# Optimization experiments

Hardware: AMD Instinct MI355X
Metric: run time of the kernel (lower is better)

## Reference

```python
import jax, jax.numpy as jnp
import numpy as np

B, T, H, W = 4, 8, 256, 256


def _shift(u, axis, d):
    """Value at index i comes from i+d along `axis`; zero (Dirichlet) boundary."""
    if d == 0:
        return u
    pad = [(0, 0)] * u.ndim
    sl = [slice(None)] * u.ndim
    if d > 0:
        sl[axis] = slice(d, None)
        pad[axis] = (0, d)
    else:
        sl[axis] = slice(None, d)
        pad[axis] = (-d, 0)
    return jnp.pad(u[tuple(sl)], pad)


def custom_sigmoid(x, mn, mx):
    # matches NLL.custom_sigmoid: (sigmoid(x) + min/(max-min)) * (max-min)
    return (jax.nn.sigmoid(x) + mn / (mx - mn)) * (mx - mn)


def setup_inputs() -> dict:
    key = jax.random.key(0)
    k1, k2 = jax.random.split(key)
    x = jax.random.normal(k1, (B, T, H, W), dtype=jnp.float32)
    conv_w = jax.random.normal(k2, (8 * T, T, 3, 3), dtype=jnp.float32) * 0.05
    return {"x": x, "conv_w": conv_w}


def reference(x, conv_w):
    Bn, Tn, Hn, Wn = x.shape
    dt = dx = dy = 1.0  # st_lag = [1,1,1]

    # Encoder: Conv2d(n_t -> 8*n_t, 3x3, padding=1, bias=False)
    theta = jax.lax.conv_general_dilated(
        x, conv_w, window_strides=(1, 1), padding="SAME",
        dimension_numbers=("NCHW", "OIHW", "NCHW"))

    # reshape_params: split 8*n_t channels into SPDE fields, bounded to valid ranges
    kappa = custom_sigmoid(theta[:, :Tn], 0.01, 1.0)          # damping
    m1 = theta[:, Tn:2 * Tn]                                   # advection x
    m2 = theta[:, 2 * Tn:3 * Tn]                               # advection y
    Hxx = custom_sigmoid(theta[:, 3 * Tn:4 * Tn], 0.01, 1.0)  # diffusion tensor
    Hxy = 0.1 * jnp.tanh(theta[:, 4 * Tn:5 * Tn])
    Hyx = 0.1 * jnp.tanh(theta[:, 5 * Tn:6 * Tn])
    Hyy = custom_sigmoid(theta[:, 6 * Tn:7 * Tn], 0.01, 1.0)
    tau = custom_sigmoid(theta[:, 7 * Tn:8 * Tn], 0.1, 10.0)   # noise scale

    # finite-difference stencils (zero Dirichlet boundary), vectorized over (B,T)
    def Dx(u):
        return (_shift(u, -1, 1) - _shift(u, -1, -1)) / (2 * dx)

    def Dy(u):
        return (_shift(u, -2, 1) - _shift(u, -2, -1)) / (2 * dy)

    def Dxx(u):
        return (_shift(u, -1, 1) + _shift(u, -1, -1) - 2 * u) / (dx * dx)

    def Dyy(u):
        return (_shift(u, -2, 1) + _shift(u, -2, -1) - 2 * u) / (dy * dy)

    def A(u):
        # advection-diffusion operator: kappa^2 u + m.grad u - div(H grad u)
        return ((kappa * kappa) * u + m1 * Dx(u) + m2 * Dy(u)
                - (Hxx * Dxx(u) + Hyy * Dyy(u) + (Hxy + Hyx) * Dx(Dy(u))))

    # pow=1 -> alpha=2 -> B = A^2 ; M_k = I + dt * B_k
    Mx = x + dt * A(A(x))                      # [B,T,H,W], M_k x_k for all k

    # Q = L^T D L with L block-bidiagonal (L[k,k]=M_k, L[k,k-1]=-I),
    # D_k = diag(dt / tau_k^2)  (inv_tau = sqrt(dt)/tau in create_Q)
    x_prev = jnp.concatenate([jnp.zeros_like(x[:, :1]), x[:, :-1]], axis=1)
    r = Mx - x_prev                            # r_k = M_k x_k - x_{k-1}
    D = dt / (tau * tau)

    xQx = jnp.sum(D * r * r)                   # quadratic form x^T Q x
    logdetD = jnp.sum(jnp.log(D))              # diagonal log-det contribution
    return 0.5 * (xQx - logdetD)
```

## Files before the change

kernel.cpp:

```cpp
#include <hip/hip_runtime.h>

#define F_ELEMS 2097152
#define IMG 65536

typedef _Float16 half8  __attribute__((ext_vector_type(8)));
typedef _Float16 half2v __attribute__((ext_vector_type(2)));
typedef _Float16 half4v __attribute__((ext_vector_type(4)));
typedef float    floatx4 __attribute__((ext_vector_type(4)));

__device__ __forceinline__ float sigm(float x){ return 1.0f/(1.0f + __expf(-x)); }
__device__ __forceinline__ float tanh_fast(float x){
    float t = __expf(2.0f*x);
    return 1.0f - 2.0f/(t + 1.0f);
}

__global__ void zero_out(float* out){ out[0] = 0.0f; }

__global__ __launch_bounds__(256) void conv_mfma(
    const float* __restrict__ x, const float* __restrict__ w,
    _Float16* __restrict__ fld, float* __restrict__ out)
{
    __shared__ _Float16 xt[4*258*8];
    __shared__ _Float16 Wl[12*64*8];
    __shared__ float red[256];

    const int tid = threadIdx.x;
    const int i0  = blockIdx.x << 1;
    const int b   = blockIdx.y;

    for (int e = tid; e < 258*4*4; e += 256){
        int cc = e % 258;
        int rr = (e/258) & 3;
        int cp = e / (258*4);
        int gi = i0 - 1 + rr, gj = cc - 1;
        float v0 = 0.0f, v1 = 0.0f;
        if (gi >= 0 && gi < 256 && gj >= 0 && gj < 256){
            int base = ((b*8 + 2*cp) << 16) + (gi << 8) + gj;
            v0 = x[base];
            v1 = x[base + IMG];
        }
        half2v h; h[0] = (_Float16)v0; h[1] = (_Float16)v1;
        *(half2v*)&xt[(rr*258 + cc)*8 + 2*cp] = h;
    }
    for (int e = tid; e < 12*64*8; e += 256){
        int c  = e & 7;
        int oc = (e >> 3) & 63;
        int t  = e >> 9;
        float v = (t < 9) ? w[(oc*8 + c)*9 + t] : 0.0f;
        Wl[e] = (_Float16)v;
    }
    __syncthreads();

    const int lane = tid & 63;
    const int quad = lane >> 4;
    const int l16  = lane & 15;
    const int wv   = tid >> 6;

    half8 afr[4][3];
    int boff[3];
    #pragma unroll
    for (int s = 0; s < 3; ++s){
        int t  = s*4 + quad;
        afr[0][s] = *(const half8*)&Wl[(t*64 +  0 + l16)*8];
        afr[1][s] = *(const half8*)&Wl[(t*64 + 16 + l16)*8];
        afr[2][s] = *(const half8*)&Wl[(t*64 + 32 + l16)*8];
        afr[3][s] = *(const half8*)&Wl[(t*64 + 48 + l16)*8];
        int tc = (t < 9) ? t : 8;
        int dh = tc / 3, dw = tc - dh*3;
        boff[s] = (dh*258 + dw)*8;
    }

    float ldacc = 0.0f;

    #pragma unroll 2
    for (int it = 0; it < 8; ++it){
        const int g   = it*4 + wv;
        const int r   = g >> 4;
        const int jb  = ((g & 15) << 4) + l16;
        const int xoff = (r*258 + jb)*8;

        floatx4 acc0 = {0,0,0,0}, acc1 = {0,0,0,0}, acc2 = {0,0,0,0}, acc3 = {0,0,0,0};
        #pragma unroll
        for (int s = 0; s < 3; ++s){
            half8 bf = *(const half8*)&xt[xoff + boff[s]];
            acc0 = __builtin_amdgcn_mfma_f32_16x16x32_f16(afr[0][s], bf, acc0, 0, 0, 0);
            acc1 = __builtin_amdgcn_mfma_f32_16x16x32_f16(afr[1][s], bf, acc1, 0, 0, 0);
            acc2 = __builtin_amdgcn_mfma_f32_16x16x32_f16(afr[2][s], bf, acc2, 0, 0, 0);
            acc3 = __builtin_amdgcn_mfma_f32_16x16x32_f16(afr[3][s], bf, acc3, 0, 0, 0);
        }

        const int pix0 = (b << 19) + ((i0 + r) << 8) + jb;
#define STO(f, tt, v) fld[(f)*F_ELEMS + ((tt) << 16) + pix0] = (_Float16)(v)
        #pragma unroll
        for (int rg = 0; rg < 4; ++rg){
            int oc = quad*4 + rg, tt = oc & 7;
            float v = acc0[rg];
            if (oc < 8){ float s = 0.99f*sigm(v) + 0.01f; STO(0, tt, s*s); }
            else       { STO(1, tt, v); }
        }
        #pragma unroll
        for (int rg = 0; rg < 4; ++rg){
            int oc = 16 + quad*4 + rg, tt = oc & 7;
            float v = acc1[rg];
            if (oc < 24){ STO(2, tt, v); }
            else        { STO(3, tt, 0.99f*sigm(v) + 0.01f); }
        }
        #pragma unroll
        for (int rg = 0; rg < 4; ++rg){
            float th    = 0.1f*tanh_fast(acc2[rg]);
            float other = __shfl_xor(th, 32, 64);
            if (quad < 2){
                int tt = quad*4 + rg;
                STO(4, tt, th + other);
            }
        }
        #pragma unroll
        for (int rg = 0; rg < 4; ++rg){
            int oc = 48 + quad*4 + rg, tt = oc & 7;
            float v = acc3[rg];
            if (oc < 56){ STO(5, tt, 0.99f*sigm(v) + 0.01f); }
            else {
                float tau = 9.9f*sigm(v) + 0.1f;
                STO(6, tt, 1.0f/(tau*tau));
                ldacc += __logf(tau);
            }
        }
#undef STO
    }

    red[tid] = ldacc;
    __syncthreads();
    for (int s = 128; s > 0; s >>= 1){
        if (tid < s) red[tid] += red[tid + s];
        __syncthreads();
    }
    if (tid == 0) atomicAdd(out, red[0]);
}

__device__ __forceinline__ void ldf4(const _Float16* __restrict__ p, float o[4]){
    half4v h = *(const half4v*)p;
    o[0] = (float)h[0]; o[1] = (float)h[1]; o[2] = (float)h[2]; o[3] = (float)h[3];
}

__device__ __forceinline__ void row6(const float* __restrict__ u, int rb, int j0, float v[6]){
    const float4 c4 = *(const float4*)&u[rb + j0];
    v[1] = c4.x; v[2] = c4.y; v[3] = c4.z; v[4] = c4.w;
    v[0] = (j0 > 0)   ? u[rb + j0 - 1] : 0.0f;
    v[5] = (j0 < 252) ? u[rb + j0 + 4] : 0.0f;
}

__device__ __forceinline__ void stencil4(const float k2[4], const float m1[4],
    const float m2[4], const float hx[4], const float hs[4], const float hy[4],
    const float vc[6], const float vn[6], const float vs[6], float rp[4])
{
    #pragma unroll
    for (int p = 0; p < 4; ++p){
        float hxx = hx[p], hyy = hy[p];
        rp[p] = (k2[p] + 2.0f*(hxx + hyy))*vc[p+1]
              + (0.5f*m1[p] - hxx)*vc[p+2]
              - (0.5f*m1[p] + hxx)*vc[p]
              + (0.5f*m2[p] - hyy)*vn[p+1]
              - (0.5f*m2[p] + hyy)*vs[p+1]
              - 0.25f*hs[p]*(vn[p+2] - vs[p+2] - vn[p] + vs[p]);
    }
}

#define YSW 268
__global__ __launch_bounds__(256) void fused_A(
    const float* __restrict__ x, const _Float16* __restrict__ fld,
    float* __restrict__ out)
{
    __shared__ float ys[18*YSW];
    __shared__ float red[256];

    const int tid = threadIdx.x;
    const int cg  = tid & 63;
    const int rw  = tid >> 6;
    const int jc  = cg << 2;
    const int bt  = blockIdx.y;
    const int t   = bt & 7;
    const int i0  = blockIdx.x << 4;

    if (tid < 18){ ys[tid*YSW + 3] = 0.0f; ys[tid*YSW + 260] = 0.0f; }

    for (int p = 0; p < 5; ++p){
        int yr = p*4 + rw;
        if (yr < 18){
            int iy = i0 - 1 + yr;
            float y[4] = {0,0,0,0};
            if (iy >= 0 && iy < 256){
                int pix = (bt << 16) + (iy << 8) + jc;
                int rb  = pix - jc;
                float vc[6], vn[6], vs[6];
                row6(x, rb, jc, vc);
                if (iy < 255) row6(x, rb + 256, jc, vn);
                else { vn[0]=vn[1]=vn[2]=vn[3]=vn[4]=vn[5]=0.0f; }
                if (iy > 0) row6(x, rb - 256, jc, vs);
                else { vs[0]=vs[1]=vs[2]=vs[3]=vs[4]=vs[5]=0.0f; }
                float k2[4], m1[4], m2[4], hx[4], hs[4], hy[4];
                ldf4(&fld[0*F_ELEMS + pix], k2);
                ldf4(&fld[1*F_ELEMS + pix], m1);
                ldf4(&fld[2*F_ELEMS + pix], m2);
                ldf4(&fld[3*F_ELEMS + pix], hx);
                ldf4(&fld[4*F_ELEMS + pix], hs);
                ldf4(&fld[5*F_ELEMS + pix], hy);
                stencil4(k2, m1, m2, hx, hs, hy, vc, vn, vs, y);
            }
            float4 y4 = make_float4(y[0], y[1], y[2], y[3]);
            *(float4*)&ys[yr*YSW + 4 + jc] = y4;
        }
    }
    __syncthreads();

    float local = 0.0f;
    #pragma unroll
    for (int p = 0; p < 4; ++p){
        int zr = p*4 + rw;
        int iz = i0 + zr;
        int pix = (bt << 16) + (iz << 8) + jc;
        int base = (zr + 1)*YSW + 4 + jc;

        float vc[6], vn[6], vs[6];
        {
            float4 c4 = *(const float4*)&ys[base];
            vc[1]=c4.x; vc[2]=c4.y; vc[3]=c4.z; vc[4]=c4.w;
            vc[0]=ys[base-1]; vc[5]=ys[base+4];
            float4 n4 = *(const float4*)&ys[base+YSW];
            vn[1]=n4.x; vn[2]=n4.y; vn[3]=n4.z; vn[4]=n4.w;
            vn[0]=ys[base+YSW-1]; vn[5]=ys[base+YSW+4];
            float4 s4 = *(const float4*)&ys[base-YSW];
            vs[1]=s4.x; vs[2]=s4.y; vs[3]=s4.z; vs[4]=s4.w;
            vs[0]=ys[base-YSW-1]; vs[5]=ys[base-YSW+4];
        }
        float k2[4], m1[4], m2[4], hx[4], hs[4], hy[4], dv[4], z[4];
        ldf4(&fld[0*F_ELEMS + pix], k2);
        ldf4(&fld[1*F_ELEMS + pix], m1);
        ldf4(&fld[2*F_ELEMS + pix], m2);
        ldf4(&fld[3*F_ELEMS + pix], hx);
        ldf4(&fld[4*F_ELEMS + pix], hs);
        ldf4(&fld[5*F_ELEMS + pix], hy);
        ldf4(&fld[6*F_ELEMS + pix], dv);
        stencil4(k2, m1, m2, hx, hs, hy, vc, vn, vs, z);

        float4 xc = *(const float4*)&x[pix];
        float4 xp = make_float4(0,0,0,0);
        if (t > 0) xp = *(const float4*)&x[pix - IMG];
        const float* xcp = (const float*)&xc;
        const float* xpp = (const float*)&xp;
        #pragma unroll
        for (int q = 0; q < 4; ++q){
            float r = xcp[q] + z[q] - xpp[q];
            local += dv[q]*r*r;
        }
    }

    red[tid] = local;
    __syncthreads();
    for (int s = 128; s > 0; s >>= 1){
        if (tid < s) red[tid] += red[tid + s];
        __syncthreads();
    }
    if (tid == 0) atomicAdd(out, 0.5f*red[0]);
}

extern "C" void kernel_launch(void* const* d_in, const int* in_sizes, int n_in,
                              void* d_out, int out_size, void* d_ws, size_t ws_size,
                              hipStream_t stream)
{
    const float* x = (const float*)d_in[0];
    const float* w = (const float*)d_in[1];
    float* out = (float*)d_out;
    _Float16* fld = (_Float16*)d_ws;

    zero_out<<<1, 1, 0, stream>>>(out);
    conv_mfma<<<dim3(128, 4), 256, 0, stream>>>(x, w, fld, out);
    fused_A<<<dim3(16, 32), 256, 0, stream>>>(x, fld, out);
}
```

Before: 108.5 us.

## Fuse conv encoder and stencil passes into one kernel with on-chip fields

Merges the MFMA convolution and the two-pass A(A(x)) stencil into a single kernel. Each block computes the conv outputs for a 4-row halo over two time slices and keeps the SPDE fields in a swizzled fp16 shared-memory layout, so the global field workspace round trip is gone. The halo rows mean the conv work is recomputed, and each block reloads weights directly from global memory. The kernel uses 512 threads and about 56KB of shared memory, which may reduce occupancy.

```diff
diff --git a/kernel.cpp b/kernel.cpp
--- a/kernel.cpp
+++ b/kernel.cpp
@@ -1,11 +1,10 @@
 #include <hip/hip_runtime.h>
 
-#define F_ELEMS 2097152
 #define IMG 65536
 
 typedef _Float16 half8  __attribute__((ext_vector_type(8)));
+typedef _Float16 half4v __attribute__((ext_vector_type(4)));
 typedef _Float16 half2v __attribute__((ext_vector_type(2)));
-typedef _Float16 half4v __attribute__((ext_vector_type(4)));
 typedef float    floatx4 __attribute__((ext_vector_type(4)));
 
 __device__ __forceinline__ float sigm(float x){ return 1.0f/(1.0f + __expf(-x)); }
@@ -13,134 +12,9 @@
     float t = __expf(2.0f*x);
     return 1.0f - 2.0f/(t + 1.0f);
 }
+__device__ __forceinline__ int swz(int px){ return px ^ ((px >> 3) & 7); }
 
 __global__ void zero_out(float* out){ out[0] = 0.0f; }
-
-__global__ __launch_bounds__(256) void conv_mfma(
-    const float* __restrict__ x, const float* __restrict__ w,
-    _Float16* __restrict__ fld, float* __restrict__ out)
-{
-    __shared__ _Float16 xt[4*258*8];
-    __shared__ _Float16 Wl[12*64*8];
-    __shared__ float red[256];
-
-    const int tid = threadIdx.x;
-    const int i0  = blockIdx.x << 1;
-    const int b   = blockIdx.y;
-
-    for (int e = tid; e < 258*4*4; e += 256){
-        int cc = e % 258;
-        int rr = (e/258) & 3;
-        int cp = e / (258*4);
-        int gi = i0 - 1 + rr, gj = cc - 1;
-        float v0 = 0.0f, v1 = 0.0f;
-        if (gi >= 0 && gi < 256 && gj >= 0 && gj < 256){
-            int base = ((b*8 + 2*cp) << 16) + (gi << 8) + gj;
-            v0 = x[base];
-            v1 = x[base + IMG];
-        }
-        half2v h; h[0] = (_Float16)v0; h[1] = (_Float16)v1;
-        *(half2v*)&xt[(rr*258 + cc)*8 + 2*cp] = h;
-    }
-    for (int e = tid; e < 12*64*8; e += 256){
-        int c  = e & 7;
-        int oc = (e >> 3) & 63;
-        int t  = e >> 9;
-        float v = (t < 9) ? w[(oc*8 + c)*9 + t] : 0.0f;
-        Wl[e] = (_Float16)v;
-    }
-    __syncthreads();
-
-    const int lane = tid & 63;
-    const int quad = lane >> 4;
-    const int l16  = lane & 15;
-    const int wv   = tid >> 6;
-
-    half8 afr[4][3];
-    int boff[3];
-    #pragma unroll
-    for (int s = 0; s < 3; ++s){
-        int t  = s*4 + quad;
-        afr[0][s] = *(const half8*)&Wl[(t*64 +  0 + l16)*8];
-        afr[1][s] = *(const half8*)&Wl[(t*64 + 16 + l16)*8];
-        afr[2][s] = *(const half8*)&Wl[(t*64 + 32 + l16)*8];
-        afr[3][s] = *(const half8*)&Wl[(t*64 + 48 + l16)*8];
-        int tc = (t < 9) ? t : 8;
-        int dh = tc / 3, dw = tc - dh*3;
-        boff[s] = (dh*258 + dw)*8;
-    }
-
-    float ldacc = 0.0f;
-
-    #pragma unroll 2
-    for (int it = 0; it < 8; ++it){
-        const int g   = it*4 + wv;
-        const int r   = g >> 4;
-        const int jb  = ((g & 15) << 4) + l16;
-        const int xoff = (r*258 + jb)*8;
-
-        floatx4 acc0 = {0,0,0,0}, acc1 = {0,0,0,0}, acc2 = {0,0,0,0}, acc3 = {0,0,0,0};
-        #pragma unroll
-        for (int s = 0; s < 3; ++s){
-            half8 bf = *(const half8*)&xt[xoff + boff[s]];
-            acc0 = __builtin_amdgcn_mfma_f32_16x16x32_f16(afr[0][s], bf, acc0, 0, 0, 0);
-            acc1 = __builtin_amdgcn_mfma_f32_16x16x32_f16(afr[1][s], bf, acc1, 0, 0, 0);
-            acc2 = __builtin_amdgcn_mfma_f32_16x16x32_f16(afr[2][s], bf, acc2, 0, 0, 0);
-            acc3 = __builtin_amdgcn_mfma_f32_16x16x32_f16(afr[3][s], bf, acc3, 0, 0, 0);
-        }
-
-        const int pix0 = (b << 19) + ((i0 + r) << 8) + jb;
-#define STO(f, tt, v) fld[(f)*F_ELEMS + ((tt) << 16) + pix0] = (_Float16)(v)
-        #pragma unroll
-        for (int rg = 0; rg < 4; ++rg){
-            int oc = quad*4 + rg, tt = oc & 7;
-            float v = acc0[rg];
-            if (oc < 8){ float s = 0.99f*sigm(v) + 0.01f; STO(0, tt, s*s); }
-            else       { STO(1, tt, v); }
-        }
-        #pragma unroll
-        for (int rg = 0; rg < 4; ++rg){
-            int oc = 16 + quad*4 + rg, tt = oc & 7;
-            float v = acc1[rg];
-            if (oc < 24){ STO(2, tt, v); }
-            else        { STO(3, tt, 0.99f*sigm(v) + 0.01f); }
-        }
-        #pragma unroll
-        for (int rg = 0; rg < 4; ++rg){
-            float th    = 0.1f*tanh_fast(acc2[rg]);
-            float other = __shfl_xor(th, 32, 64);
-            if (quad < 2){
-                int tt = quad*4 + rg;
-                STO(4, tt, th + other);
-            }
-        }
-        #pragma unroll
-        for (int rg = 0; rg < 4; ++rg){
-            int oc = 48 + quad*4 + rg, tt = oc & 7;
-            float v = acc3[rg];
-            if (oc < 56){ STO(5, tt, 0.99f*sigm(v) + 0.01f); }
-            else {
-                float tau = 9.9f*sigm(v) + 0.1f;
-                STO(6, tt, 1.0f/(tau*tau));
-                ldacc += __logf(tau);
-            }
-        }
-#undef STO
-    }
-
-    red[tid] = ldacc;
-    __syncthreads();
-    for (int s = 128; s > 0; s >>= 1){
-        if (tid < s) red[tid] += red[tid + s];
-        __syncthreads();
-    }
-    if (tid == 0) atomicAdd(out, red[0]);
-}
-
-__device__ __forceinline__ void ldf4(const _Float16* __restrict__ p, float o[4]){
-    half4v h = *(const half4v*)p;
-    o[0] = (float)h[0]; o[1] = (float)h[1]; o[2] = (float)h[2]; o[3] = (float)h[3];
-}
 
 __device__ __forceinline__ void row6(const float* __restrict__ u, int rb, int j0, float v[6]){
     const float4 c4 = *(const float4*)&u[rb + j0];
@@ -148,7 +22,9 @@
     v[0] = (j0 > 0)   ? u[rb + j0 - 1] : 0.0f;
     v[5] = (j0 < 252) ? u[rb + j0 + 4] : 0.0f;
 }
-
+__device__ __forceinline__ void zero6(float v[6]){
+    v[0]=v[1]=v[2]=v[3]=v[4]=v[5]=0.0f;
+}
 __device__ __forceinline__ void stencil4(const float k2[4], const float m1[4],
     const float m2[4], const float hx[4], const float hs[4], const float hy[4],
     const float vc[6], const float vn[6], const float vs[6], float rp[4])
@@ -165,82 +41,168 @@
     }
 }
 
-#define YSW 268
-__global__ __launch_bounds__(256) void fused_A(
-    const float* __restrict__ x, const _Float16* __restrict__ fld,
+__global__ __launch_bounds__(512) void fused_all(
+    const float* __restrict__ x, const float* __restrict__ w,
     float* __restrict__ out)
 {
-    __shared__ float ys[18*YSW];
-    __shared__ float red[256];
-
-    const int tid = threadIdx.x;
-    const int cg  = tid & 63;
-    const int rw  = tid >> 6;
-    const int jc  = cg << 2;
-    const int bt  = blockIdx.y;
-    const int t   = bt & 7;
-    const int i0  = blockIdx.x << 4;
-
-    if (tid < 18){ ys[tid*YSW + 3] = 0.0f; ys[tid*YSW + 260] = 0.0f; }
-
-    for (int p = 0; p < 5; ++p){
-        int yr = p*4 + rw;
-        if (yr < 18){
-            int iy = i0 - 1 + yr;
-            float y[4] = {0,0,0,0};
-            if (iy >= 0 && iy < 256){
-                int pix = (bt << 16) + (iy << 8) + jc;
-                int rb  = pix - jc;
-                float vc[6], vn[6], vs[6];
-                row6(x, rb, jc, vc);
-                if (iy < 255) row6(x, rb + 256, jc, vn);
-                else { vn[0]=vn[1]=vn[2]=vn[3]=vn[4]=vn[5]=0.0f; }
-                if (iy > 0) row6(x, rb - 256, jc, vs);
-                else { vs[0]=vs[1]=vs[2]=vs[3]=vs[4]=vs[5]=0.0f; }
-                float k2[4], m1[4], m2[4], hx[4], hs[4], hy[4];
-                ldf4(&fld[0*F_ELEMS + pix], k2);
-                ldf4(&fld[1*F_ELEMS + pix], m1);
-                ldf4(&fld[2*F_ELEMS + pix], m2);
-                ldf4(&fld[3*F_ELEMS + pix], hx);
-                ldf4(&fld[4*F_ELEMS + pix], hs);
-                ldf4(&fld[5*F_ELEMS + pix], hy);
-                stencil4(k2, m1, m2, hx, hs, hy, vc, vn, vs, y);
+    __shared__ __align__(16) unsigned char smem[24768 + 32768];
+    _Float16* xt  = (_Float16*)smem;
+    _Float16* fl  = (_Float16*)(smem + 24768);
+    float*    ys  = (float*)smem;
+    float*    red = (float*)(smem + 8576);
+
+    const int tid  = threadIdx.x;
+    const int lane = tid & 63;
+    const int wv   = tid >> 6;
+    const int l16  = lane & 15;
+    const int quad = lane >> 4;
+    const int i0   = blockIdx.x << 1;
+    const int b    = blockIdx.y >> 2;
+    const int tp   = blockIdx.y & 3;
+
+    for (int e = tid; e < 6*4*258; e += 512){
+        int cc = e % 258;
+        int q  = e / 258;
+        int rr = q >> 2;
+        int cp = q & 3;
+        int gi = i0 - 2 + rr, gj = cc - 1;
+        float v0 = 0.0f, v1 = 0.0f;
+        if ((unsigned)gi < 256u && (unsigned)gj < 256u){
+            int base = (((b << 3) + (cp << 1)) << 16) + (gi << 8) + gj;
+            v0 = x[base];
+            v1 = x[base + IMG];
+        }
+        half2v h; h[0] = (_Float16)v0; h[1] = (_Float16)v1;
+        *(half2v*)&xt[(rr*258 + cc)*8 + (cp << 1)] = h;
+    }
+
+    half8 afr[3];
+    int boff[3];
+    {
+        int oc = ((l16 & 7) << 3) + (tp << 1) + (l16 >> 3);
+        #pragma unroll
+        for (int s = 0; s < 3; ++s){
+            int tap = s*4 + quad;
+            half8 a;
+            if (tap < 9){
+                #pragma unroll
+                for (int j = 0; j < 8; ++j)
+                    a[j] = (_Float16)w[(oc*8 + j)*9 + tap];
+                int dh = tap/3, dw = tap - dh*3;
+                boff[s] = (dh*258 + dw)*8;
+            } else {
+                #pragma unroll
+                for (int j = 0; j < 8; ++j) a[j] = (_Float16)0.0f;
+                boff[s] = 0;
             }
-            float4 y4 = make_float4(y[0], y[1], y[2], y[3]);
-            *(float4*)&ys[yr*YSW + 4 + jc] = y4;
-        }
+            afr[s] = a;
+        }
+    }
+    __syncthreads();
+
+    float ldacc = 0.0f;
+    #pragma unroll
+    for (int it = 0; it < 8; ++it){
+        int g  = it*8 + wv;
+        int ry = g >> 4;
+        int jb = ((g & 15) << 4) + l16;
+        int base = (ry*258 + jb)*8;
+        floatx4 acc = {0,0,0,0};
+        #pragma unroll
+        for (int s = 0; s < 3; ++s){
+            half8 bf = *(const half8*)&xt[base + boff[s]];
+            acc = __builtin_amdgcn_mfma_f32_16x16x32_f16(afr[s], bf, acc, 0, 0, 0);
+        }
+        int tl    = quad >> 1;
+        int flidx = ((((ry << 1) + tl) << 8) + swz(jb)) << 3;
+        half4v v;
+        if ((quad & 1) == 0){
+            float s0 = 0.99f*sigm(acc[0]) + 0.01f;
+            v[0] = (_Float16)(s0*s0);
+            v[1] = (_Float16)acc[1];
+            v[2] = (_Float16)acc[2];
+            v[3] = (_Float16)(0.99f*sigm(acc[3]) + 0.01f);
+            *(half4v*)&fl[flidx] = v;
+        } else {
+            float hs  = 0.1f*(tanh_fast(acc[0]) + tanh_fast(acc[1]));
+            float hyy = 0.99f*sigm(acc[2]) + 0.01f;
+            float tau = 9.9f*sigm(acc[3]) + 0.1f;
+            v[0] = (_Float16)hs;
+            v[1] = (_Float16)0.0f;
+            v[2] = (_Float16)hyy;
+            v[3] = (_Float16)(1.0f/(tau*tau));
+            *(half4v*)&fl[flidx + 4] = v;
+            if ((unsigned)(ry - 1) <= 1u)
+                ldacc += __logf(tau);
+        }
+    }
+    __syncthreads();
+
+    if (tid < 16){
+        int tl = tid >> 3, row = (tid >> 1) & 3, side = tid & 1;
+        ys[(tl*4 + row)*268 + (side ? 260 : 3)] = 0.0f;
+    }
+    {
+        int tl  = tid >> 8;
+        int row = (tid >> 6) & 3;
+        int cg  = tid & 63;
+        int jc  = cg << 2;
+        int gi  = i0 - 1 + row;
+        float4 y4 = make_float4(0,0,0,0);
+        if ((unsigned)gi < 256u){
+            int bt  = (b << 3) + (tp << 1) + tl;
+            int pix = (bt << 16) + (gi << 8) + jc;
+            int rb  = pix - jc;
+            float vc[6], vn[6], vs[6];
+            row6(x, rb, jc, vc);
+            if (gi < 255) row6(x, rb + 256, jc, vn); else zero6(vn);
+            if (gi > 0)   row6(x, rb - 256, jc, vs); else zero6(vs);
+            float k2[4], m1[4], m2[4], hx[4], hsv[4], hy[4], yv[4];
+            #pragma unroll
+            for (int p = 0; p < 4; ++p){
+                half8 f8 = *(const half8*)&fl[(((((row << 1) + tl) << 8) + swz(jc + p)) << 3)];
+                k2[p]=(float)f8[0]; m1[p]=(float)f8[1]; m2[p]=(float)f8[2];
+                hx[p]=(float)f8[3]; hsv[p]=(float)f8[4]; hy[p]=(float)f8[6];
+            }
+            stencil4(k2, m1, m2, hx, hsv, hy, vc, vn, vs, yv);
+            y4 = make_float4(yv[0], yv[1], yv[2], yv[3]);
+        }
+        *(float4*)&ys[(tl*4 + row)*268 + 4 + jc] = y4;
     }
     __syncthreads();
 
     float local = 0.0f;
-    #pragma unroll
-    for (int p = 0; p < 4; ++p){
-        int zr = p*4 + rw;
-        int iz = i0 + zr;
-        int pix = (bt << 16) + (iz << 8) + jc;
-        int base = (zr + 1)*YSW + 4 + jc;
+    if (tid < 256){
+        int tl = tid >> 7;
+        int zr = (tid >> 6) & 1;
+        int cg = tid & 63;
+        int jc = cg << 2;
+        int gi = i0 + zr;
+        int t  = (tp << 1) + tl;
+        int pix = (((b << 3) + t) << 16) + (gi << 8) + jc;
+        int yb  = (tl*4 + zr + 1)*268 + 4 + jc;
 
         float vc[6], vn[6], vs[6];
         {
-            float4 c4 = *(const float4*)&ys[base];
+            float4 c4 = *(const float4*)&ys[yb];
             vc[1]=c4.x; vc[2]=c4.y; vc[3]=c4.z; vc[4]=c4.w;
-            vc[0]=ys[base-1]; vc[5]=ys[base+4];
-            float4 n4 = *(const float4*)&ys[base+YSW];
+            vc[0]=ys[yb-1]; vc[5]=ys[yb+4];
+            float4 n4 = *(const float4*)&ys[yb+268];
             vn[1]=n4.x; vn[2]=n4.y; vn[3]=n4.z; vn[4]=n4.w;
-            vn[0]=ys[base+YSW-1]; vn[5]=ys[base+YSW+4];
-            float4 s4 = *(const float4*)&ys[base-YSW];
+            vn[0]=ys[yb+268-1]; vn[5]=ys[yb+268+4];
+            float4 s4 = *(const float4*)&ys[yb-268];
             vs[1]=s4.x; vs[2]=s4.y; vs[3]=s4.z; vs[4]=s4.w;
-            vs[0]=ys[base-YSW-1]; vs[5]=ys[base-YSW+4];
-        }
-        float k2[4], m1[4], m2[4], hx[4], hs[4], hy[4], dv[4], z[4];
-        ldf4(&fld[0*F_ELEMS + pix], k2);
-        ldf4(&fld[1*F_ELEMS + pix], m1);
-        ldf4(&fld[2*F_ELEMS + pix], m2);
-        ldf4(&fld[3*F_ELEMS + pix], hx);
-        ldf4(&fld[4*F_ELEMS + pix], hs);
-        ldf4(&fld[5*F_ELEMS + pix], hy);
-        ldf4(&fld[6*F_ELEMS + pix], dv);
-        stencil4(k2, m1, m2, hx, hs, hy, vc, vn, vs, z);
+            vs[0]=ys[yb-268-1]; vs[5]=ys[yb-268+4];
+        }
+        float k2[4], m1[4], m2[4], hx[4], hsv[4], hy[4], dv[4], zv[4];
+        #pragma unroll
+        for (int p = 0; p < 4; ++p){
+            half8 f8 = *(const half8*)&fl[((((((zr + 1) << 1) + tl) << 8) + swz(jc + p)) << 3)];
+            k2[p]=(float)f8[0]; m1[p]=(float)f8[1]; m2[p]=(float)f8[2];
+            hx[p]=(float)f8[3]; hsv[p]=(float)f8[4]; hy[p]=(float)f8[6];
+            dv[p]=(float)f8[7];
+        }
+        stencil4(k2, m1, m2, hx, hsv, hy, vc, vn, vs, zv);
 
         float4 xc = *(const float4*)&x[pix];
         float4 xp = make_float4(0,0,0,0);
@@ -249,18 +211,18 @@
         const float* xpp = (const float*)&xp;
         #pragma unroll
         for (int q = 0; q < 4; ++q){
-            float r = xcp[q] + z[q] - xpp[q];
+            float r = xcp[q] + zv[q] - xpp[q];
             local += dv[q]*r*r;
         }
     }
 
-    red[tid] = local;
-    __syncthreads();
-    for (int s = 128; s > 0; s >>= 1){
+    red[tid] = 0.5f*local + ldacc;
+    __syncthreads();
+    for (int s = 256; s > 0; s >>= 1){
         if (tid < s) red[tid] += red[tid + s];
         __syncthreads();
     }
-    if (tid == 0) atomicAdd(out, 0.5f*red[0]);
+    if (tid == 0) atomicAdd(out, red[0]);
 }
 
 extern "C" void kernel_launch(void* const* d_in, const int* in_sizes, int n_in,
@@ -270,9 +232,7 @@
     const float* x = (const float*)d_in[0];
     const float* w = (const float*)d_in[1];
     float* out = (float*)d_out;
-    _Float16* fld = (_Float16*)d_ws;
 
     zero_out<<<1, 1, 0, stream>>>(out);
-    conv_mfma<<<dim3(128, 4), 256, 0, stream>>>(x, w, fld, out);
-    fused_A<<<dim3(16, 32), 256, 0, stream>>>(x, fld, out);
-}
+    fused_all<<<dim3(128, 16), 512, 0, stream>>>(x, w, out);
+}
```

Result: slower. 132.8 us (+22.4%).
